# Performance work log

Hardware: AMD Instinct MI355X
Metric: run time of the kernel (lower is better)

The kernel has to match this reference:

```python
import jax, jax.numpy as jnp
import numpy as np

D_MODEL = 1024
D_STATE = 64
T, B = 512, 8
DECAY_INIT = 3.0


def _xavier(key, fan_in, fan_out):
    lim = float(np.sqrt(6.0 / (fan_in + fan_out)))
    return jax.random.uniform(key, (fan_in, fan_out), jnp.float32, -lim, lim)


def setup_inputs() -> dict:
    key = jax.random.key(0)
    ks = jax.random.split(key, 8)
    x = jax.random.normal(ks[0], (T, B, D_MODEL), jnp.float32)
    z = jax.random.normal(ks[1], (T, B, D_MODEL), jnp.float32)
    H0 = jnp.zeros((B, D_MODEL, D_STATE), jnp.float32)
    # weights stored as [in, out] so projection is x @ W + b
    Wk = _xavier(ks[2], D_MODEL, D_MODEL)
    bk = jnp.zeros((D_MODEL,), jnp.float32)
    Wv = _xavier(ks[3], D_MODEL, D_STATE)
    bv = jnp.zeros((D_STATE,), jnp.float32)
    Wq = _xavier(ks[4], D_MODEL, D_STATE)
    bq = jnp.zeros((D_STATE,), jnp.float32)
    Wd = jnp.zeros((D_MODEL, D_MODEL), jnp.float32)  # zero-init per _init_weights
    bd = jnp.full((D_MODEL,), DECAY_INIT, jnp.float32)
    return {"x": x, "z": z, "H0": H0, "Wk": Wk, "bk": bk, "Wv": Wv, "bv": bv,
            "Wq": Wq, "bq": bq, "Wd": Wd, "bd": bd}


def reference(x, z, H0, Wk, bk, Wv, bv, Wq, bq, Wd, bd):
    # Precompute all per-timestep projections in parallel: [T,B,*]
    key = jnp.tanh(jnp.einsum('tbd,de->tbe', x, Wk) + bk)       # [T,B,d]
    value = jnp.einsum('tbd,dk->tbk', x, Wv) + bv                # [T,B,k]
    decay = jax.nn.sigmoid(jnp.einsum('tbd,de->tbe', x, Wd) + bd)  # [T,B,d]
    query = jnp.einsum('tbd,dk->tbk', x, Wq) + bq                # [T,B,k]

    def step(H, inp):
        k_t, v_t, d_t, q_t, z_t = inp
        H_new = d_t[:, :, None] * H + k_t[:, :, None] * v_t[:, None, :]  # [B,d,k]
        pre_out = jnp.einsum('bdk,bk->bd', H_new, q_t)                   # [B,d]
        out = pre_out * jax.nn.silu(z_t)
        return H_new, (out, H_new)

    _, (output, Hs) = jax.lax.scan(step, H0, (key, value, decay, query, z))
    H_all = jnp.concatenate([H0[None], Hs], axis=0)  # [T+1,B,d,k]
    return output, H_all
```

## Files before the change

### kernel.cpp

```cpp
#include <hip/hip_runtime.h>
#include <stdint.h>

#define TSTEPS 512
#define BATCH 8
#define DM 1024
#define DK 64
#define MROWS (TSTEPS*BATCH)
#define NCAT 2176
#define NCHUNK 16
#define CLEN 32

typedef __attribute__((ext_vector_type(8))) __bf16 bf16x8;
typedef __attribute__((ext_vector_type(4))) float f32x4;

__device__ __forceinline__ unsigned short f2bf(float f) {
  unsigned int u = __float_as_uint(f);
  u += 0x7fffu + ((u >> 16) & 1u);
  return (unsigned short)(u >> 16);
}

__global__ __launch_bounds__(256) void k_prep(const float* __restrict__ x,
                                              ushort* __restrict__ xb,
                                              const float* __restrict__ Wk,
                                              const float* __restrict__ Wd,
                                              const float* __restrict__ Wv,
                                              const float* __restrict__ Wq,
                                              ushort* __restrict__ Wcat,
                                              const float* __restrict__ bk,
                                              const float* __restrict__ bdc,
                                              const float* __restrict__ bv,
                                              const float* __restrict__ bq,
                                              float* __restrict__ biasc) {
  __shared__ float s[32][33];
  int bid = blockIdx.x, tid = threadIdx.x;
  if (bid < 2048) {
    int i = bid * 256 + tid;
    const float4* x4 = (const float4*)x;
    float4 a = x4[2*i], b = x4[2*i+1];
    union { ushort ss[8]; uint4 v; } o;
    o.ss[0]=f2bf(a.x); o.ss[1]=f2bf(a.y); o.ss[2]=f2bf(a.z); o.ss[3]=f2bf(a.w);
    o.ss[4]=f2bf(b.x); o.ss[5]=f2bf(b.y); o.ss[6]=f2bf(b.z); o.ss[7]=f2bf(b.w);
    ((uint4*)xb)[i] = o.v;
    return;
  }
  if (bid < 4224) {
    const float* src; int rel, lg, rowOff;
    size_t N;
    if (bid < 3072)      { src = Wk; N = 1024; lg = 5; rowOff = 0;    rel = bid - 2048; }
    else if (bid < 4096) { src = Wd; N = 1024; lg = 5; rowOff = 1024; rel = bid - 3072; }
    else if (bid < 4160) { src = Wv; N = 64;   lg = 1; rowOff = 2048; rel = bid - 4096; }
    else                 { src = Wq; N = 64;   lg = 1; rowOff = 2112; rel = bid - 4160; }
    int n0 = (rel & ((1 << lg) - 1)) << 5;
    int k0 = (rel >> lg) << 5;
    int tx = tid & 31, ty = tid >> 5;
    for (int i = 0; i < 4; ++i)
      s[ty + 8*i][tx] = src[(size_t)(k0 + ty + 8*i) * N + n0 + tx];
    __syncthreads();
    for (int i = 0; i < 4; ++i)
      Wcat[(size_t)(n0 + ty + 8*i + rowOff) * 1024 + k0 + tx] = f2bf(s[tx][ty + 8*i]);
    return;
  }
  int n = (bid - 4224) * 256 + tid;
  if (n >= NCAT) return;
  float v;
  if (n < 1024)      v = bk[n];
  else if (n < 2048) v = bdc[n - 1024];
  else if (n < 2112) v = bv[n - 2048];
  else               v = bq[n - 2112];
  biasc[n] = v;
}


__global__ __launch_bounds__(256) void k_gemm(const ushort* __restrict__ A,
                                              const ushort* __restrict__ Bt,
                                              const float* __restrict__ bias,
                                              float* __restrict__ C) {
  __shared__ ushort As[128*64];
  __shared__ ushort Bs[128*64];
  int tid = threadIdx.x;
  int w = tid >> 6, l = tid & 63;
  int m0 = blockIdx.y * 128, n0 = blockIdx.x * 128;
  int wr = w >> 1, wc = w & 1;
  f32x4 acc[4][4] = {};
  int srow = w*8 + (l >> 3);
  int scol = (l & 7) * 8;
  int lr = l & 15, lk8 = (l >> 4) * 8;
  for (int k0 = 0; k0 < 1024; k0 += 64) {
    __syncthreads();
    for (int r = 0; r < 4; ++r) {
      __builtin_amdgcn_global_load_lds(
        (const __attribute__((address_space(1))) void*)(A + (size_t)(m0 + r*32 + srow)*1024 + k0 + scol),
        (__attribute__((address_space(3))) void*)(As + r*2048 + w*512), 16, 0, 0);
      __builtin_amdgcn_global_load_lds(
        (const __attribute__((address_space(1))) void*)(Bt + (size_t)(n0 + r*32 + srow)*1024 + k0 + scol),
        (__attribute__((address_space(3))) void*)(Bs + r*2048 + w*512), 16, 0, 0);
    }
    __syncthreads();
    for (int kk = 0; kk < 64; kk += 32) {
      bf16x8 af[4], bfr[4];
#pragma unroll
      for (int i = 0; i < 4; ++i)
        af[i] = *(const bf16x8*)(As + (wr*64 + i*16 + lr)*64 + kk + lk8);
#pragma unroll
      for (int j = 0; j < 4; ++j)
        bfr[j] = *(const bf16x8*)(Bs + (wc*64 + j*16 + lr)*64 + kk + lk8);
#pragma unroll
      for (int i = 0; i < 4; ++i)
#pragma unroll
        for (int j = 0; j < 4; ++j)
          acc[i][j] = __builtin_amdgcn_mfma_f32_16x16x32_bf16(af[i], bfr[j], acc[i][j], 0, 0, 0);
    }
  }
  int epi = (blockIdx.x < 8) ? 0 : ((blockIdx.x < 16) ? 1 : 2);
#pragma unroll
  for (int i = 0; i < 4; ++i)
#pragma unroll
    for (int j = 0; j < 4; ++j) {
      int col = n0 + wc*64 + j*16 + lr;
      int row0 = m0 + wr*64 + i*16 + (l >> 4)*4;
      float bs = bias[col];
#pragma unroll
      for (int r = 0; r < 4; ++r) {
        float v = acc[i][j][r] + bs;
        if (epi == 0)      v = tanhf(v);
        else if (epi == 1) v = 1.0f/(1.0f + expf(-v));
        C[(size_t)(row0 + r)*NCAT + col] = v;
      }
    }
}


__global__ __launch_bounds__(256) void k_phase1(const float* __restrict__ C,
                                                float* __restrict__ Sws,
                                                float* __restrict__ Dp) {
  int bid = blockIdx.x;
  int c = bid >> 9, b = (bid >> 6) & 7, dg = bid & 63;
  int tid = threadIdx.x;
  int d = dg*16 + (tid >> 4), kq = tid & 15;
  f32x4 h = {};
  float dp = 1.0f;
  for (int tl = 0; tl < CLEN; ++tl) {
    int t = c*CLEN + tl;
    const float* Crow = C + ((size_t)t*BATCH + b)*NCAT;
    float de = Crow[1024 + d];
    float ke = Crow[d];
    f32x4 v = ((const f32x4*)(Crow + 2048))[kq];
    h = de*h + ke*v;
    dp *= de;
  }
  ((f32x4*)Sws)[(size_t)c*131072 + ((size_t)b*DM + d)*16 + kq] = h;
  if (kq == 0) Dp[(size_t)(c*BATCH + b)*DM + d] = dp;
}

__global__ __launch_bounds__(256) void k_phase2(const float* __restrict__ H0,
                                                const float* __restrict__ Dp,
                                                float* __restrict__ Sws) {
  int q = blockIdx.x*256 + threadIdx.x;
  int bd = q >> 4;
  f32x4 h = ((const f32x4*)H0)[q];
  f32x4* S4 = (f32x4*)Sws;
  for (int c = 0; c < NCHUNK - 1; ++c) {
    float dp = Dp[(size_t)c*BATCH*DM + bd];
    size_t idx = (size_t)c*131072 + q;
    h = dp*h + S4[idx];
    S4[idx] = h;
  }
}

__global__ __launch_bounds__(256) void k_phase3(const float* __restrict__ C,
                                                const float* __restrict__ z,
                                                const float* __restrict__ H0,
                                                const float* __restrict__ Sws,
                                                float* __restrict__ out,
                                                float* __restrict__ Hall) {
  int bid = blockIdx.x;
  int c = bid >> 9, b = (bid >> 6) & 7, dg = bid & 63;
  int tid = threadIdx.x;
  int d = dg*16 + (tid >> 4), kq = tid & 15;
  size_t bd16 = ((size_t)b*DM + d)*16 + kq;
  f32x4 h = (c == 0) ? ((const f32x4*)H0)[bd16]
                     : ((const f32x4*)Sws)[(size_t)(c-1)*131072 + bd16];
  f32x4* H4 = (f32x4*)Hall;
  if (c == 0) __builtin_nontemporal_store(h, &H4[bd16]);
  for (int tl = 0; tl < CLEN; ++tl) {
    int t = c*CLEN + tl;
    size_t row = (size_t)t*BATCH + b;
    const float* Crow = C + row*NCAT;
    float de = Crow[1024 + d];
    float ke = Crow[d];
    f32x4 v = ((const f32x4*)(Crow + 2048))[kq];
    f32x4 q = ((const f32x4*)(Crow + 2048))[16 + kq];
    h = de*h + ke*v;
    float s = h[0]*q[0] + h[1]*q[1] + h[2]*q[2] + h[3]*q[3];
    s += __shfl_xor(s, 1, 16);
    s += __shfl_xor(s, 2, 16);
    s += __shfl_xor(s, 4, 16);
    s += __shfl_xor(s, 8, 16);
    if (kq == 0) {
      float zz = z[row*DM + d];
      float sig = 1.0f/(1.0f + __expf(-zz));
      out[row*DM + d] = s * zz * sig;
    }
    __builtin_nontemporal_store(h, &H4[(size_t)(t+1)*131072 + bd16]);
  }
}


extern "C" void kernel_launch(void* const* d_in, const int* in_sizes, int n_in,
                              void* d_out, int out_size, void* d_ws, size_t ws_size,
                              hipStream_t stream) {
  const float* x  = (const float*)d_in[0];
  const float* z  = (const float*)d_in[1];
  const float* H0 = (const float*)d_in[2];
  const float* Wk = (const float*)d_in[3];
  const float* bk = (const float*)d_in[4];
  const float* Wv = (const float*)d_in[5];
  const float* bv = (const float*)d_in[6];
  const float* Wq = (const float*)d_in[7];
  const float* bq = (const float*)d_in[8];
  const float* Wd = (const float*)d_in[9];
  const float* bd = (const float*)d_in[10];

  float* out  = (float*)d_out;
  float* Hall = out + (size_t)TSTEPS*BATCH*DM;

  char* ws = (char*)d_ws;
  size_t off = 0;
  ushort* xb   = (ushort*)(ws + off); off += (size_t)MROWS*DM*2;
  ushort* Wcat = (ushort*)(ws + off); off += (size_t)NCAT*DM*2;
  float* biasc = (float*)(ws + off);  off += (size_t)NCAT*4; off = (off + 255) & ~(size_t)255;
  float* C     = (float*)(ws + off);  off += (size_t)MROWS*NCAT*4;
  float* Sws   = (float*)(ws + off);  off += (size_t)NCHUNK*BATCH*DM*DK*4;
  float* Dp    = (float*)(ws + off);  off += (size_t)NCHUNK*BATCH*DM*4;
  if (off > ws_size) return;

  k_prep<<<4233, 256, 0, stream>>>(x, xb, Wk, Wd, Wv, Wq, Wcat, bk, bd, bv, bq, biasc);
  k_gemm<<<dim3(17,32), 256, 0, stream>>>(xb, Wcat, biasc, C);
  k_phase1<<<(NCHUNK-1)*BATCH*64, 256, 0, stream>>>(C, Sws, Dp);
  k_phase2<<<512, 256, 0, stream>>>(H0, Dp, Sws);
  k_phase3<<<NCHUNK*BATCH*64, 256, 0, stream>>>(C, z, H0, Sws, out, Hall);
}
```

Baseline: 297.8 us.

## Replace chunked scan phases 1-2 with single sequential scan kernel

```diff
diff --git a/kernel.cpp b/kernel.cpp
--- a/kernel.cpp
+++ b/kernel.cpp
@@ -129,41 +129,26 @@
     }
 }
 
-
-__global__ __launch_bounds__(256) void k_phase1(const float* __restrict__ C,
-                                                float* __restrict__ Sws,
-                                                float* __restrict__ Dp) {
+__global__ __launch_bounds__(256) void k_scan(const float* __restrict__ C,
+                                              const float* __restrict__ H0,
+                                              float* __restrict__ Sws) {
   int bid = blockIdx.x;
-  int c = bid >> 9, b = (bid >> 6) & 7, dg = bid & 63;
+  int b = bid >> 6, dg = bid & 63;
   int tid = threadIdx.x;
   int d = dg*16 + (tid >> 4), kq = tid & 15;
-  f32x4 h = {};
-  float dp = 1.0f;
-  for (int tl = 0; tl < CLEN; ++tl) {
-    int t = c*CLEN + tl;
-    const float* Crow = C + ((size_t)t*BATCH + b)*NCAT;
-    float de = Crow[1024 + d];
-    float ke = Crow[d];
-    f32x4 v = ((const f32x4*)(Crow + 2048))[kq];
-    h = de*h + ke*v;
-    dp *= de;
-  }
-  ((f32x4*)Sws)[(size_t)c*131072 + ((size_t)b*DM + d)*16 + kq] = h;
-  if (kq == 0) Dp[(size_t)(c*BATCH + b)*DM + d] = dp;
-}
-
-__global__ __launch_bounds__(256) void k_phase2(const float* __restrict__ H0,
-                                                const float* __restrict__ Dp,
-                                                float* __restrict__ Sws) {
-  int q = blockIdx.x*256 + threadIdx.x;
-  int bd = q >> 4;
-  f32x4 h = ((const f32x4*)H0)[q];
-  f32x4* S4 = (f32x4*)Sws;
-  for (int c = 0; c < NCHUNK - 1; ++c) {
-    float dp = Dp[(size_t)c*BATCH*DM + bd];
-    size_t idx = (size_t)c*131072 + q;
-    h = dp*h + S4[idx];
-    S4[idx] = h;
+  size_t bd16 = ((size_t)b*DM + d)*16 + kq;
+  f32x4 h = ((const f32x4*)H0)[bd16];
+  for (int c = 0; c < NCHUNK-1; ++c) {
+#pragma unroll 4
+    for (int tl = 0; tl < CLEN; ++tl) {
+      int t = c*CLEN + tl;
+      const float* Crow = C + ((size_t)t*BATCH + b)*NCAT;
+      float de = Crow[1024 + d];
+      float ke = Crow[d];
+      f32x4 v = ((const f32x4*)(Crow + 2048))[kq];
+      h = de*h + ke*v;
+    }
+    ((f32x4*)Sws)[(size_t)c*131072 + bd16] = h;
   }
 }
 
@@ -181,7 +166,7 @@
   f32x4 h = (c == 0) ? ((const f32x4*)H0)[bd16]
                      : ((const f32x4*)Sws)[(size_t)(c-1)*131072 + bd16];
   f32x4* H4 = (f32x4*)Hall;
-  if (c == 0) __builtin_nontemporal_store(h, &H4[bd16]);
+  if (c == 0) H4[bd16] = h;
   for (int tl = 0; tl < CLEN; ++tl) {
     int t = c*CLEN + tl;
     size_t row = (size_t)t*BATCH + b;
@@ -201,7 +186,7 @@
       float sig = 1.0f/(1.0f + __expf(-zz));
       out[row*DM + d] = s * zz * sig;
     }
-    __builtin_nontemporal_store(h, &H4[(size_t)(t+1)*131072 + bd16]);
+    H4[(size_t)(t+1)*131072 + bd16] = h;
   }
 }
 
@@ -230,13 +215,11 @@
   ushort* Wcat = (ushort*)(ws + off); off += (size_t)NCAT*DM*2;
   float* biasc = (float*)(ws + off);  off += (size_t)NCAT*4; off = (off + 255) & ~(size_t)255;
   float* C     = (float*)(ws + off);  off += (size_t)MROWS*NCAT*4;
-  float* Sws   = (float*)(ws + off);  off += (size_t)NCHUNK*BATCH*DM*DK*4;
-  float* Dp    = (float*)(ws + off);  off += (size_t)NCHUNK*BATCH*DM*4;
+  float* Sws   = (float*)(ws + off);  off += (size_t)(NCHUNK-1)*BATCH*DM*DK*4;
   if (off > ws_size) return;
 
   k_prep<<<4233, 256, 0, stream>>>(x, xb, Wk, Wd, Wv, Wq, Wcat, bk, bd, bv, bq, biasc);
   k_gemm<<<dim3(17,32), 256, 0, stream>>>(xb, Wcat, biasc, C);
-  k_phase1<<<(NCHUNK-1)*BATCH*64, 256, 0, stream>>>(C, Sws, Dp);
-  k_phase2<<<512, 256, 0, stream>>>(H0, Dp, Sws);
+  k_scan<<<512, 256, 0, stream>>>(C, H0, Sws);
   k_phase3<<<NCHUNK*BATCH*64, 256, 0, stream>>>(C, z, H0, Sws, out, Hall);
 }
```

Result: slower. 455.2 us (+52.8%).
